# Performance work log

Hardware: AMD Instinct MI355X
Metric: run time of the kernel (lower is better)

## Reference

```python
import jax, jax.numpy as jnp
import numpy as np

NUM_HEADS = 12
THETA = 10000.0


def _rope(x, pos):
    # x: [B, H, S, dk]; interleaved even/odd pair rotation
    dk = x.shape[-1]
    freqs = THETA ** (-jnp.arange(dk // 2, dtype=jnp.float32) * 2.0 / dk)  # [dk/2]
    ang = pos.astype(jnp.float32)[:, None] * freqs                         # [S, dk/2]
    cos, sin = jnp.cos(ang), jnp.sin(ang)
    x1, x2 = x[..., 0::2], x[..., 1::2]
    rot = jnp.stack([x1 * cos - x2 * sin, x1 * sin + x2 * cos], axis=-1)
    return rot.reshape(x.shape)


def setup_inputs() -> dict:
    key = jax.random.key(0)
    ks = jax.random.split(key, 5)
    B, S, D = 4, 2048, 768
    w_scale = 1.0 / np.sqrt(D).astype(np.float32)
    x = jax.random.normal(ks[0], (B, S, D), dtype=jnp.float32)
    Wq = jax.random.normal(ks[1], (D, D), dtype=jnp.float32) * w_scale
    Wk = jax.random.normal(ks[2], (D, D), dtype=jnp.float32) * w_scale
    Wv = jax.random.normal(ks[3], (D, D), dtype=jnp.float32) * w_scale
    Wo = jax.random.normal(ks[4], (D, D), dtype=jnp.float32) * w_scale
    token_positions = jnp.arange(S, dtype=jnp.int32)
    return {"x": x, "Wq": Wq, "Wk": Wk, "Wv": Wv, "Wo": Wo,
            "token_positions": token_positions}


def reference(x, Wq, Wk, Wv, Wo, token_positions):
    B, S, D = x.shape
    H = NUM_HEADS
    dk = D // H
    # bias-free linear layers: y = x @ W^T (torch Linear weight convention)
    q = (x @ Wq.T).reshape(B, S, H, dk).transpose(0, 2, 1, 3)  # [B,H,S,dk]
    k = (x @ Wk.T).reshape(B, S, H, dk).transpose(0, 2, 1, 3)
    v = (x @ Wv.T).reshape(B, S, H, dk).transpose(0, 2, 1, 3)
    q = _rope(q, token_positions)
    k = _rope(k, token_positions)
    scores = jnp.einsum('bhqd,bhkd->bhqk', q, k) / np.float32(np.sqrt(dk))
    causal = jnp.tril(jnp.ones((S, S), dtype=bool))
    scores = jnp.where(causal, scores, -jnp.inf)
    attn = jax.nn.softmax(scores, axis=-1)                      # [B,H,S,S]
    out = jnp.einsum('bhqk,bhkd->bhqd', attn, v)
    out = out.transpose(0, 2, 1, 3).reshape(B, S, D)
    return out @ Wo.T
```

## Files before the change

kernel.cpp:

```cpp
#include <hip/hip_runtime.h>
#include <cstdint>
#include <cstddef>

#define NTOK 8192
#define SLEN 2048
#define DM   768
#define NH   12
#define DKH  64

typedef __attribute__((ext_vector_type(8))) short bf16x8;
typedef __attribute__((ext_vector_type(4))) float f32x4;

__device__ __forceinline__ float b2f(unsigned short u) {
  return __uint_as_float(((unsigned)u) << 16);
}
__device__ __forceinline__ unsigned short f2b(float f) {
  unsigned u = __float_as_uint(f);
  u += 0x7fffu + ((u >> 16) & 1u);
  return (unsigned short)(u >> 16);
}
__device__ __forceinline__ unsigned cvtpk(float lo, float hi) {
  unsigned r;
  asm("v_cvt_pk_bf16_f32 %0, %1, %2" : "=v"(r) : "v"(lo), "v"(hi));
  return r;
}

__device__ __forceinline__ void gld16(const void* g, void* l) {
  __builtin_amdgcn_global_load_lds(
      (const __attribute__((address_space(1))) void*)g,
      (__attribute__((address_space(3))) void*)l, 16, 0, 0);
}

#define BAR_DRAIN() do {                                  \
    asm volatile("s_waitcnt vmcnt(0)" ::: "memory");      \
    __builtin_amdgcn_s_barrier();                         \
    __builtin_amdgcn_sched_barrier(0);                    \
  } while (0)
#define BAR_KEEP4() do {                                  \
    asm volatile("s_waitcnt vmcnt(4)" ::: "memory");      \
    __builtin_amdgcn_s_barrier();                         \
    __builtin_amdgcn_sched_barrier(0);                    \
  } while (0)

__global__ void cast_bf16_kernel(const float* __restrict__ in,
                                 unsigned short* __restrict__ out, int n8) {
  int i = blockIdx.x * blockDim.x + threadIdx.x;
  if (i >= n8) return;
  const float4* p = (const float4*)(in + (size_t)i * 8);
  float4 a = p[0], b = p[1];
  union { unsigned short h[8]; bf16x8 v; } u;
  u.h[0] = f2b(a.x); u.h[1] = f2b(a.y); u.h[2] = f2b(a.z); u.h[3] = f2b(a.w);
  u.h[4] = f2b(b.x); u.h[5] = f2b(b.y); u.h[6] = f2b(b.z); u.h[7] = f2b(b.w);
  *(bf16x8*)(out + (size_t)i * 8) = u.v;
}

__global__ void cast4_bf16_kernel(const float* __restrict__ s0,
                                  const float* __restrict__ s1,
                                  const float* __restrict__ s2,
                                  const float* __restrict__ s3,
                                  unsigned short* __restrict__ out, int n8) {
  int i = blockIdx.x * blockDim.x + threadIdx.x;
  if (i >= n8) return;
  const float* src = (blockIdx.y == 0) ? s0 : (blockIdx.y == 1) ? s1
                    : (blockIdx.y == 2) ? s2 : s3;
  unsigned short* o = out + (size_t)blockIdx.y * DM * DM + (size_t)i * 8;
  const float4* p = (const float4*)(src + (size_t)i * 8);
  float4 a = p[0], b = p[1];
  union { unsigned short h[8]; bf16x8 v; } u;
  u.h[0] = f2b(a.x); u.h[1] = f2b(a.y); u.h[2] = f2b(a.z); u.h[3] = f2b(a.w);
  u.h[4] = f2b(b.x); u.h[5] = f2b(b.y); u.h[6] = f2b(b.z); u.h[7] = f2b(b.w);
  *(bf16x8*)o = u.v;
}

__device__ __forceinline__ void stv(float* p, float v) { *p = v; }
__device__ __forceinline__ void stv(unsigned short* p, float v) { *p = f2b(v); }

template <typename CT>
__global__ __launch_bounds__(256, 2) void gemm_bt_kernel(
    const unsigned short* __restrict__ A,
    const unsigned short* __restrict__ B0, const unsigned short* __restrict__ B1,
    const unsigned short* __restrict__ B2,
    CT* __restrict__ C0, CT* __restrict__ C1, CT* __restrict__ C2,
    int N, int K, const int* __restrict__ pos, int do_rope) {
  const unsigned short* Bp = (blockIdx.z == 0) ? B0 : (blockIdx.z == 1) ? B1 : B2;
  CT* Cp = (blockIdx.z == 0) ? C0 : (blockIdx.z == 1) ? C1 : C2;
  const int tid = threadIdx.x, wid = tid >> 6, lane = tid & 63;
  const int lrow = lane & 15, lk8 = (lane >> 4) << 3;
  const int m0 = blockIdx.y * 128, n0 = blockIdx.x * 128;
  const int wm = (wid >> 1) * 64, wn = (wid & 1) * 64;
  const int sr = lane >> 3, sc = (lane & 7) * 8;
  __shared__ unsigned short At[2][128 * 64];
  __shared__ unsigned short Bt[2][128 * 64];
  f32x4 acc[4][4] = {};

  auto stage = [&](int kk, int buf) {
    const int k0 = kk * 64;
#pragma unroll
    for (int i = 0; i < 4; ++i) {
      int r = (wid * 4 + i) * 8 + sr;
      int k = sc ^ ((r & 7) << 3);
      gld16(A  + (size_t)(m0 + r) * K + k0 + k, &At[buf][(wid * 4 + i) * 512]);
      gld16(Bp + (size_t)(n0 + r) * K + k0 + k, &Bt[buf][(wid * 4 + i) * 512]);
    }
  };

  const int nk = K / 64;
  stage(0, 0);
  BAR_DRAIN();
  for (int kk = 0; kk < nk; ++kk) {
    const int cur = kk & 1;
    if (kk + 1 < nk) stage(kk + 1, cur ^ 1);
    bf16x8 af[2][4], bfr[2][4];
#pragma unroll
    for (int ks = 0; ks < 2; ++ks)
#pragma unroll
      for (int mi = 0; mi < 4; ++mi) {
        int ra = wm + mi * 16 + lrow;
        af[ks][mi]  = *(const bf16x8*)&At[cur][ra * 64 + ((ks * 32 + lk8) ^ ((ra & 7) << 3))];
        int rb = wn + mi * 16 + lrow;
        bfr[ks][mi] = *(const bf16x8*)&Bt[cur][rb * 64 + ((ks * 32 + lk8) ^ ((rb & 7) << 3))];
      }
#pragma unroll
    for (int ks = 0; ks < 2; ++ks)
#pragma unroll
      for (int mi = 0; mi < 4; ++mi)
#pragma unroll
        for (int ni = 0; ni < 4; ++ni)
          acc[mi][ni] = __builtin_amdgcn_mfma_f32_16x16x32_bf16(
              af[ks][mi], bfr[ks][ni], acc[mi][ni], 0, 0, 0);
    BAR_DRAIN();
  }

  const bool ropeq = do_rope && (blockIdx.z < 2);
  if (ropeq) {
    float frq[4];
#pragma unroll
    for (int ni = 0; ni < 4; ++ni)
      frq[ni] = exp2f((float)(((n0 + wn + ni * 16 + lrow) & 63) >> 1) *
                      -0.4152410118609203f);
#pragma unroll
    for (int mi = 0; mi < 4; ++mi)
#pragma unroll
      for (int r = 0; r < 4; ++r) {
        int row = m0 + wm + mi * 16 + (lane >> 4) * 4 + r;
        float ps = (float)pos[row & (SLEN - 1)];
#pragma unroll
        for (int ni = 0; ni < 4; ++ni) {
          float v = acc[mi][ni][r];
          float prt = __shfl_xor(v, 1);
          float sn, cs;
          __sincosf(ps * frq[ni], &sn, &cs);
          acc[mi][ni][r] = (lrow & 1) ? fmaf(prt, sn, v * cs)
                                      : fmaf(v, cs, -prt * sn);
        }
      }
  }

#pragma unroll
  for (int mi = 0; mi < 4; ++mi)
#pragma unroll
    for (int ni = 0; ni < 4; ++ni)
#pragma unroll
      for (int r = 0; r < 4; ++r) {
        int row = m0 + wm + mi * 16 + (lane >> 4) * 4 + r;
        int col = n0 + wn + ni * 16 + lrow;
        stv(Cp + (size_t)row * N + col, acc[mi][ni][r]);
      }
}

__global__ void transpose_v_kernel(const unsigned short* __restrict__ V,
                                   unsigned short* __restrict__ VT) {
  const int tt = blockIdx.x, bh = blockIdx.y;
  const int b = bh / NH, h = bh - b * NH;
  const unsigned short* src = V + ((size_t)b * SLEN + tt * 64) * DM + h * DKH;
  unsigned short* dst = VT + (size_t)bh * DKH * SLEN + tt * 64;
  __shared__ unsigned short lds[64][72];
  const int tid = threadIdx.x;
  const int r = tid >> 2, cq = tid & 3;
#pragma unroll
  for (int pass = 0; pass < 2; ++pass) {
    int c = cq * 8 + pass * 32;
    *(bf16x8*)&lds[r][c] = *(const bf16x8*)&src[(size_t)r * DM + c];
  }
  __syncthreads();
  const int d = tid >> 2;
#pragma unroll
  for (int pass = 0; pass < 2; ++pass) {
    int s0 = cq * 8 + pass * 32;
    union { unsigned short h[8]; bf16x8 v; } o;
#pragma unroll
    for (int j = 0; j < 8; ++j) {
      int pi = pass * 32 + 16 * (j >> 2) + 4 * cq + (j & 3);
      o.h[j] = lds[pi][d];
    }
    *(bf16x8*)&dst[(size_t)d * SLEN + s0] = o.v;
  }
}

__global__ __launch_bounds__(256, 2) void attn_kernel(
    const unsigned short* __restrict__ Q, const unsigned short* __restrict__ Kg,
    const unsigned short* __restrict__ VT, unsigned short* __restrict__ O) {
  const int bh = blockIdx.x;
  const int qt = 15 - (int)blockIdx.y;
  const int b = bh / NH, h = bh - b * NH;
  const size_t base = ((size_t)b * SLEN) * DM + h * DKH;
  const size_t vbase = (size_t)bh * DKH * SLEN;
  const int tid = threadIdx.x, wid = tid >> 6, lane = tid & 63;
  const int lrow = lane & 15, g = lane >> 4;

  __shared__ unsigned short Kt[3][64 * 64];
  __shared__ unsigned short Vt[3][64 * 64];

  bf16x8 qf[2][2];
#pragma unroll
  for (int mi = 0; mi < 2; ++mi)
#pragma unroll
    for (int ks = 0; ks < 2; ++ks) {
      const int qrow = qt * 128 + wid * 32 + mi * 16 + lrow;
      union { unsigned short h[8]; bf16x8 v; } u;
      u.v = *(const bf16x8*)&Q[base + (size_t)qrow * DM + ks * 32 + g * 8];
#pragma unroll
      for (int j = 0; j < 8; ++j)
        u.h[j] = f2b(b2f(u.h[j]) * 0.18033688011112042f);
      qf[mi][ks] = u.v;
    }

  f32x4 oacc[2][4] = {};
  float m_run[2] = {-1e30f, -1e30f};
  float l_part[2] = {0.f, 0.f};
  const int qg0 = qt * 128 + wid * 32 + lrow;
  const int nkt = 2 * qt + 2;

  const int srow = wid * 8 + (lane >> 3);
  const int scol = (lane & 7) * 8;

  auto stage = [&](int kt, int buf) {
#pragma unroll
    for (int rnd = 0; rnd < 2; ++rnd) {
      int r = rnd * 32 + srow;
      int c = scol ^ ((r & 7) << 3);
      gld16(Kg + base + (size_t)(kt * 64 + r) * DM + c,
            &Kt[buf][(rnd * 32 + wid * 8) * 64]);
    }
#pragma unroll
    for (int rnd = 0; rnd < 2; ++rnd) {
      int d = rnd * 32 + srow;
      int c = scol ^ ((d & 7) << 3);
      gld16(VT + vbase + (size_t)d * SLEN + kt * 64 + c,
            &Vt[buf][(rnd * 32 + wid * 8) * 64]);
    }
  };

  auto compute = [&](int kt, int buf) {
    const bool active = !(kt == 2 * qt + 1 && wid < 2);
    if (!active) return;
    f32x4 sa[2][4] = {};
    const unsigned short* Ks = Kt[buf];
    __builtin_amdgcn_s_setprio(1);
#pragma unroll
    for (int ks = 0; ks < 2; ++ks)
#pragma unroll
      for (int ni = 0; ni < 4; ++ni) {
        const int krow = ni * 16 + lrow;
        bf16x8 kf = *(const bf16x8*)
            &Ks[krow * 64 + ((ks * 32 + g * 8) ^ ((krow & 7) << 3))];
#pragma unroll
        for (int mi = 0; mi < 2; ++mi)
          sa[mi][ni] = __builtin_amdgcn_mfma_f32_16x16x32_bf16(
              kf, qf[mi][ks], sa[mi][ni], 0, 0, 0);
      }
    __builtin_amdgcn_s_setprio(0);

    const bool need_mask = (kt * 64 + 64 > qt * 128 + wid * 32);
    if (need_mask) {
      const int kb = kt * 64 + g * 4;
#pragma unroll
      for (int mi = 0; mi < 2; ++mi) {
        const int qg = qg0 + mi * 16;
#pragma unroll
        for (int ni = 0; ni < 4; ++ni)
#pragma unroll
          for (int r = 0; r < 4; ++r)
            if (kb + ni * 16 + r > qg) sa[mi][ni][r] = -1e30f;
      }
    }

    float mx[2];
#pragma unroll
    for (int mi = 0; mi < 2; ++mi) {
      f32x4 t01, t23;
#pragma unroll
      for (int r = 0; r < 4; ++r) {
        t01[r] = fmaxf(sa[mi][0][r], sa[mi][1][r]);
        t23[r] = fmaxf(sa[mi][2][r], sa[mi][3][r]);
      }
      float a = fmaxf(fmaxf(t01[0], t23[0]), fmaxf(t01[1], t23[1]));
      float c = fmaxf(fmaxf(t01[2], t23[2]), fmaxf(t01[3], t23[3]));
      mx[mi] = fmaxf(a, c);
    }

    const int viol = (mx[0] > m_run[0] + 8.f) || (mx[1] > m_run[1] + 8.f);
    if (__any(viol)) {
#pragma unroll
      for (int mi = 0; mi < 2; ++mi) {
        float mr = fmaxf(mx[mi], __shfl_xor(mx[mi], 16));
        mr = fmaxf(mr, __shfl_xor(mr, 32));
        float mn = fmaxf(m_run[mi], mr);
        float scl = exp2f(m_run[mi] - mn);
        m_run[mi] = mn;
        l_part[mi] *= scl;
#pragma unroll
        for (int ni = 0; ni < 4; ++ni) oacc[mi][ni] *= scl;
      }
    }

#pragma unroll
    for (int mi = 0; mi < 2; ++mi) {
      float s0 = 0.f;
#pragma unroll
      for (int ni = 0; ni < 4; ++ni)
#pragma unroll
        for (int r = 0; r < 4; ++r) {
          float e = exp2f(sa[mi][ni][r] - m_run[mi]);
          sa[mi][ni][r] = e;
          s0 += e;
        }
      l_part[mi] += s0;
    }

    bf16x8 pf[2][2];
#pragma unroll
    for (int mi = 0; mi < 2; ++mi)
#pragma unroll
      for (int ks = 0; ks < 2; ++ks) {
        union { unsigned u[4]; bf16x8 v; } uu;
        uu.u[0] = cvtpk(sa[mi][2 * ks][0],     sa[mi][2 * ks][1]);
        uu.u[1] = cvtpk(sa[mi][2 * ks][2],     sa[mi][2 * ks][3]);
        uu.u[2] = cvtpk(sa[mi][2 * ks + 1][0], sa[mi][2 * ks + 1][1]);
        uu.u[3] = cvtpk(sa[mi][2 * ks + 1][2], sa[mi][2 * ks + 1][3]);
        pf[mi][ks] = uu.v;
      }

    const unsigned short* Vs = Vt[buf];
    __builtin_amdgcn_s_setprio(1);
#pragma unroll
    for (int ks = 0; ks < 2; ++ks)
#pragma unroll
      for (int ni = 0; ni < 4; ++ni) {
        const int d = ni * 16 + lrow;
        bf16x8 vf = *(const bf16x8*)
            &Vs[d * 64 + ((ks * 32 + g * 8) ^ ((d & 7) << 3))];
#pragma unroll
        for (int mi = 0; mi < 2; ++mi)
          oacc[mi][ni] = __builtin_amdgcn_mfma_f32_16x16x32_bf16(
              vf, pf[mi][ks], oacc[mi][ni], 0, 0, 0);
      }
    __builtin_amdgcn_s_setprio(0);
  };

  stage(0, 0);
  for (int kt = 0; kt < nkt; ++kt) {
    if (kt + 1 < nkt) {
      stage(kt + 1, (kt + 1) % 3);
      BAR_KEEP4();
    } else {
      BAR_DRAIN();
    }
    compute(kt, kt % 3);
  }

#pragma unroll
  for (int mi = 0; mi < 2; ++mi) {
    float l = l_part[mi];
    l += __shfl_xor(l, 16);
    l += __shfl_xor(l, 32);
    const float inv = 1.f / l;
    const int qrow = qt * 128 + wid * 32 + mi * 16 + lrow;
#pragma unroll
    for (int ni = 0; ni < 4; ++ni) {
      union { unsigned u[2]; ushort4 s; } o;
      o.u[0] = cvtpk(oacc[mi][ni][0] * inv, oacc[mi][ni][1] * inv);
      o.u[1] = cvtpk(oacc[mi][ni][2] * inv, oacc[mi][ni][3] * inv);
      *(ushort4*)&O[base + (size_t)qrow * DM + ni * 16 + g * 4] = o.s;
    }
  }
}

extern "C" void kernel_launch(void* const* d_in, const int* in_sizes, int n_in,
                              void* d_out, int out_size, void* d_ws, size_t ws_size,
                              hipStream_t stream) {
  const float* x  = (const float*)d_in[0];
  const float* Wq = (const float*)d_in[1];
  const float* Wk = (const float*)d_in[2];
  const float* Wv = (const float*)d_in[3];
  const float* Wo = (const float*)d_in[4];
  const int* pos  = (const int*)d_in[5];
  float* out = (float*)d_out;

  char* ws = (char*)d_ws;
  size_t off = 0;
  auto carve = [&](size_t bytes) -> void* {
    void* p = ws + off;
    off += (bytes + 255) & ~(size_t)255;
    return p;
  };
  unsigned short* xb  = (unsigned short*)carve((size_t)NTOK * DM * 2);
  unsigned short* wqb = (unsigned short*)carve((size_t)DM * DM * 2);
  unsigned short* wkb = (unsigned short*)carve((size_t)DM * DM * 2);
  unsigned short* wvb = (unsigned short*)carve((size_t)DM * DM * 2);
  unsigned short* wob = (unsigned short*)carve((size_t)DM * DM * 2);
  unsigned short* Qb  = (unsigned short*)carve((size_t)NTOK * DM * 2);
  unsigned short* Kb  = (unsigned short*)carve((size_t)NTOK * DM * 2);
  unsigned short* Vb  = (unsigned short*)carve((size_t)NTOK * DM * 2);
  unsigned short* Ab  = (unsigned short*)carve((size_t)NTOK * DM * 2);
  unsigned short* VTb = (unsigned short*)carve((size_t)4 * NH * DKH * SLEN * 2);

  const int n8x = NTOK * DM / 8;
  const int n8w = DM * DM / 8;
  cast_bf16_kernel<<<dim3((n8x + 255) / 256), dim3(256), 0, stream>>>(x, xb, n8x);
  cast4_bf16_kernel<<<dim3((n8w + 255) / 256, 4), dim3(256), 0, stream>>>(
      Wq, Wk, Wv, Wo, wqb, n8w);

  gemm_bt_kernel<unsigned short><<<dim3(6, 64, 3), dim3(256), 0, stream>>>(
      xb, wqb, wkb, wvb, Qb, Kb, Vb, DM, DM, pos, 1);

  transpose_v_kernel<<<dim3(SLEN / 64, 4 * NH), dim3(256), 0, stream>>>(Vb, VTb);

  attn_kernel<<<dim3(48, 16), dim3(256), 0, stream>>>(Qb, Kb, VTb, Ab);

  gemm_bt_kernel<float><<<dim3(6, 64, 1), dim3(256), 0, stream>>>(
      Ab, wob, wob, wob, out, out, out, DM, DM, pos, 0);
}
```

Before: 146.3 us.

## Single-buffer GEMM with transposed MFMA output, vector stores, MFMA row-sum in attention

The projection GEMM drops its double-buffered async LDS pipeline in favour of a single buffer with two __syncthreads per k-step. MFMA operands are swapped so each lane holds four consecutive columns, which lets RoPE rotate pairs inside a lane without shuffles and lets outputs go out as vector stores. In attention, the softmax denominator is now accumulated by an extra MFMA against a ones vector instead of scalar adds plus cross-lane shuffles. Losing the double buffer exposes global-load latency in the GEMM, and the extra MFMAs add matrix work to the attention loop.

```diff
diff --git a/kernel.cpp b/kernel.cpp
--- a/kernel.cpp
+++ b/kernel.cpp
@@ -72,9 +72,6 @@
   *(bf16x8*)o = u.v;
 }
 
-__device__ __forceinline__ void stv(float* p, float v) { *p = v; }
-__device__ __forceinline__ void stv(unsigned short* p, float v) { *p = f2b(v); }
-
 template <typename CT>
 __global__ __launch_bounds__(256, 2) void gemm_bt_kernel(
     const unsigned short* __restrict__ A,
@@ -85,40 +82,32 @@
   const unsigned short* Bp = (blockIdx.z == 0) ? B0 : (blockIdx.z == 1) ? B1 : B2;
   CT* Cp = (blockIdx.z == 0) ? C0 : (blockIdx.z == 1) ? C1 : C2;
   const int tid = threadIdx.x, wid = tid >> 6, lane = tid & 63;
-  const int lrow = lane & 15, lk8 = (lane >> 4) << 3;
+  const int lrow = lane & 15, g = lane >> 4, lk8 = g * 8;
   const int m0 = blockIdx.y * 128, n0 = blockIdx.x * 128;
   const int wm = (wid >> 1) * 64, wn = (wid & 1) * 64;
   const int sr = lane >> 3, sc = (lane & 7) * 8;
-  __shared__ unsigned short At[2][128 * 64];
-  __shared__ unsigned short Bt[2][128 * 64];
+  __shared__ unsigned short At[128 * 64];
+  __shared__ unsigned short Bt[128 * 64];
   f32x4 acc[4][4] = {};
-
-  auto stage = [&](int kk, int buf) {
-    const int k0 = kk * 64;
+  for (int k0 = 0; k0 < K; k0 += 64) {
+    __syncthreads();
 #pragma unroll
     for (int i = 0; i < 4; ++i) {
       int r = (wid * 4 + i) * 8 + sr;
       int k = sc ^ ((r & 7) << 3);
-      gld16(A  + (size_t)(m0 + r) * K + k0 + k, &At[buf][(wid * 4 + i) * 512]);
-      gld16(Bp + (size_t)(n0 + r) * K + k0 + k, &Bt[buf][(wid * 4 + i) * 512]);
-    }
-  };
-
-  const int nk = K / 64;
-  stage(0, 0);
-  BAR_DRAIN();
-  for (int kk = 0; kk < nk; ++kk) {
-    const int cur = kk & 1;
-    if (kk + 1 < nk) stage(kk + 1, cur ^ 1);
+      gld16(A  + (size_t)(m0 + r) * K + k0 + k, &At[(wid * 4 + i) * 512]);
+      gld16(Bp + (size_t)(n0 + r) * K + k0 + k, &Bt[(wid * 4 + i) * 512]);
+    }
+    __syncthreads();
     bf16x8 af[2][4], bfr[2][4];
 #pragma unroll
     for (int ks = 0; ks < 2; ++ks)
 #pragma unroll
       for (int mi = 0; mi < 4; ++mi) {
         int ra = wm + mi * 16 + lrow;
-        af[ks][mi]  = *(const bf16x8*)&At[cur][ra * 64 + ((ks * 32 + lk8) ^ ((ra & 7) << 3))];
+        af[ks][mi]  = *(const bf16x8*)&At[ra * 64 + ((ks * 32 + lk8) ^ ((ra & 7) << 3))];
         int rb = wn + mi * 16 + lrow;
-        bfr[ks][mi] = *(const bf16x8*)&Bt[cur][rb * 64 + ((ks * 32 + lk8) ^ ((rb & 7) << 3))];
+        bfr[ks][mi] = *(const bf16x8*)&Bt[rb * 64 + ((ks * 32 + lk8) ^ ((rb & 7) << 3))];
       }
 #pragma unroll
     for (int ks = 0; ks < 2; ++ks)
@@ -127,45 +116,52 @@
 #pragma unroll
         for (int ni = 0; ni < 4; ++ni)
           acc[mi][ni] = __builtin_amdgcn_mfma_f32_16x16x32_bf16(
-              af[ks][mi], bfr[ks][ni], acc[mi][ni], 0, 0, 0);
-    BAR_DRAIN();
+              bfr[ks][ni], af[ks][mi], acc[mi][ni], 0, 0, 0);
   }
 
   const bool ropeq = do_rope && (blockIdx.z < 2);
   if (ropeq) {
-    float frq[4];
+    float frq[4][2];
 #pragma unroll
     for (int ni = 0; ni < 4; ++ni)
-      frq[ni] = exp2f((float)(((n0 + wn + ni * 16 + lrow) & 63) >> 1) *
-                      -0.4152410118609203f);
-#pragma unroll
-    for (int mi = 0; mi < 4; ++mi)
-#pragma unroll
-      for (int r = 0; r < 4; ++r) {
-        int row = m0 + wm + mi * 16 + (lane >> 4) * 4 + r;
-        float ps = (float)pos[row & (SLEN - 1)];
-#pragma unroll
-        for (int ni = 0; ni < 4; ++ni) {
-          float v = acc[mi][ni][r];
-          float prt = __shfl_xor(v, 1);
+#pragma unroll
+      for (int rp = 0; rp < 2; ++rp)
+        frq[ni][rp] = exp2f(
+            (float)(((wn + ni * 16 + g * 4 + rp * 2) & 63) >> 1) *
+            -0.4152410118609203f);
+#pragma unroll
+    for (int mi = 0; mi < 4; ++mi) {
+      const int m = m0 + wm + mi * 16 + lrow;
+      const float ps = (float)pos[m & (SLEN - 1)];
+#pragma unroll
+      for (int ni = 0; ni < 4; ++ni)
+#pragma unroll
+        for (int rp = 0; rp < 2; ++rp) {
           float sn, cs;
-          __sincosf(ps * frq[ni], &sn, &cs);
-          acc[mi][ni][r] = (lrow & 1) ? fmaf(prt, sn, v * cs)
-                                      : fmaf(v, cs, -prt * sn);
+          __sincosf(ps * frq[ni][rp], &sn, &cs);
+          float x1 = acc[mi][ni][2 * rp], x2 = acc[mi][ni][2 * rp + 1];
+          acc[mi][ni][2 * rp]     = fmaf(x1, cs, -x2 * sn);
+          acc[mi][ni][2 * rp + 1] = fmaf(x1, sn, x2 * cs);
         }
-      }
-  }
-
-#pragma unroll
-  for (int mi = 0; mi < 4; ++mi)
-#pragma unroll
-    for (int ni = 0; ni < 4; ++ni)
-#pragma unroll
-      for (int r = 0; r < 4; ++r) {
-        int row = m0 + wm + mi * 16 + (lane >> 4) * 4 + r;
-        int col = n0 + wn + ni * 16 + lrow;
-        stv(Cp + (size_t)row * N + col, acc[mi][ni][r]);
-      }
+    }
+  }
+
+#pragma unroll
+  for (int mi = 0; mi < 4; ++mi) {
+    const int m = m0 + wm + mi * 16 + lrow;
+#pragma unroll
+    for (int ni = 0; ni < 4; ++ni) {
+      const int nb = n0 + wn + ni * 16 + g * 4;
+      if constexpr (sizeof(CT) == 2) {
+        union { unsigned u[2]; ushort4 s; } o;
+        o.u[0] = cvtpk(acc[mi][ni][0], acc[mi][ni][1]);
+        o.u[1] = cvtpk(acc[mi][ni][2], acc[mi][ni][3]);
+        *(ushort4*)&Cp[(size_t)m * N + nb] = o.s;
+      } else {
+        *(f32x4*)&Cp[(size_t)m * N + nb] = acc[mi][ni];
+      }
+    }
+  }
 }
 
 __global__ void transpose_v_kernel(const unsigned short* __restrict__ V,
@@ -225,9 +221,14 @@
       qf[mi][ks] = u.v;
     }
 
+  union { unsigned short h[8]; bf16x8 v; } one_u;
+#pragma unroll
+  for (int j = 0; j < 8; ++j) one_u.h[j] = 0x3F80;
+  const bf16x8 ones = one_u.v;
+
   f32x4 oacc[2][4] = {};
+  f32x4 l_acc[2] = {};
   float m_run[2] = {-1e30f, -1e30f};
-  float l_part[2] = {0.f, 0.f};
   const int qg0 = qt * 128 + wid * 32 + lrow;
   const int nkt = 2 * qt + 2;
 
@@ -308,25 +309,19 @@
         float mn = fmaxf(m_run[mi], mr);
         float scl = exp2f(m_run[mi] - mn);
         m_run[mi] = mn;
-        l_part[mi] *= scl;
+        l_acc[mi] *= scl;
 #pragma unroll
         for (int ni = 0; ni < 4; ++ni) oacc[mi][ni] *= scl;
       }
     }
 
 #pragma unroll
-    for (int mi = 0; mi < 2; ++mi) {
-      float s0 = 0.f;
+    for (int mi = 0; mi < 2; ++mi)
 #pragma unroll
       for (int ni = 0; ni < 4; ++ni)
 #pragma unroll
-        for (int r = 0; r < 4; ++r) {
-          float e = exp2f(sa[mi][ni][r] - m_run[mi]);
-          sa[mi][ni][r] = e;
-          s0 += e;
-        }
-      l_part[mi] += s0;
-    }
+        for (int r = 0; r < 4; ++r)
+          sa[mi][ni][r] = exp2f(sa[mi][ni][r] - m_run[mi]);
 
     bf16x8 pf[2][2];
 #pragma unroll
@@ -344,7 +339,7 @@
     const unsigned short* Vs = Vt[buf];
     __builtin_amdgcn_s_setprio(1);
 #pragma unroll
-    for (int ks = 0; ks < 2; ++ks)
+    for (int ks = 0; ks < 2; ++ks) {
 #pragma unroll
       for (int ni = 0; ni < 4; ++ni) {
         const int d = ni * 16 + lrow;
@@ -355,6 +350,11 @@
           oacc[mi][ni] = __builtin_amdgcn_mfma_f32_16x16x32_bf16(
               vf, pf[mi][ks], oacc[mi][ni], 0, 0, 0);
       }
+#pragma unroll
+      for (int mi = 0; mi < 2; ++mi)
+        l_acc[mi] = __builtin_amdgcn_mfma_f32_16x16x32_bf16(
+            ones, pf[mi][ks], l_acc[mi], 0, 0, 0);
+    }
     __builtin_amdgcn_s_setprio(0);
   };
 
@@ -371,10 +371,7 @@
 
 #pragma unroll
   for (int mi = 0; mi < 2; ++mi) {
-    float l = l_part[mi];
-    l += __shfl_xor(l, 16);
-    l += __shfl_xor(l, 32);
-    const float inv = 1.f / l;
+    const float inv = 1.f / l_acc[mi][0];
     const int qrow = qt * 128 + wid * 32 + mi * 16 + lrow;
 #pragma unroll
     for (int ni = 0; ni < 4; ++ni) {
```

Measured after the change: 140.2 us. 1.04x faster.
